# Kernel optimization log

Hardware: AMD Instinct MI355X
Metric: run time of the kernel (lower is better)

Reference implementation:

```python
import jax, jax.numpy as jnp
import numpy as np

EMBED_DIM = 1024
NUM_HEADS = 16
HEAD_DIM = EMBED_DIM // NUM_HEADS
ROPE_BASE = 10000.0


def rotate_half(x):
    # interleaved variant: pairs (x0,x1) -> (-x1, x0)
    x1 = x[..., ::2]
    x2 = x[..., 1::2]
    return jnp.stack((-x2, x1), axis=-1).reshape(x.shape)


def rope_tables(T, dim, dtype):
    inv_freq = 1.0 / (ROPE_BASE ** (jnp.arange(0, dim, 2, dtype=jnp.float32) / dim))
    t = jnp.arange(T, dtype=jnp.float32)
    freqs = t[:, None] * inv_freq[None, :]          # [T, dim/2]
    emb = jnp.concatenate((freqs, freqs), axis=-1)  # [T, dim]
    return jnp.cos(emb).astype(dtype), jnp.sin(emb).astype(dtype)


def setup_inputs() -> dict:
    key = jax.random.key(0)
    kx, kq, ko = jax.random.split(key, 3)
    B, T, D = 2, 2048, EMBED_DIM
    x = jax.random.normal(kx, (B, T, D), dtype=jnp.float32)
    s = 1.0 / np.sqrt(D)
    Wqkv = jax.random.normal(kq, (D, 3 * D), dtype=jnp.float32) * s
    Wout = jax.random.normal(ko, (D, D), dtype=jnp.float32) * s
    return {"x": x, "Wqkv": Wqkv, "Wout": Wout}


def reference(x, Wqkv, Wout):
    B, T, D = x.shape
    H, hd = NUM_HEADS, HEAD_DIM
    qkv = x @ Wqkv                                   # [B,T,3D]
    q, k, v = jnp.split(qkv, 3, axis=-1)
    q = q.reshape(B, T, H, hd).transpose(0, 2, 1, 3)  # [B,H,T,hd]
    k = k.reshape(B, T, H, hd).transpose(0, 2, 1, 3)
    v = v.reshape(B, T, H, hd).transpose(0, 2, 1, 3)
    cos, sin = rope_tables(T, hd, x.dtype)           # [T,hd]
    cos = cos[None, None, :, :]
    sin = sin[None, None, :, :]
    q = q * cos + rotate_half(q) * sin
    k = k * cos + rotate_half(k) * sin
    scale = 1.0 / np.sqrt(hd).astype(np.float32)
    attn = jnp.einsum('bhtd,bhsd->bhts', q, k) * scale  # [B,H,T,T]
    attn = jax.nn.softmax(attn, axis=-1)
    out = jnp.einsum('bhts,bhsd->bhtd', attn, v)     # [B,H,T,hd]
    out = out.transpose(0, 2, 1, 3).reshape(B, T, D)
    return out @ Wout
```

## Files before the change

kernel.cpp:

```cpp
#include <hip/hip_runtime.h>
#include <hip/hip_bf16.h>
#include <stdint.h>


typedef unsigned short u16;
typedef short bf16x8 __attribute__((ext_vector_type(8)));
typedef float f32x4  __attribute__((ext_vector_type(4)));

#if defined(__has_builtin) && __has_builtin(__builtin_amdgcn_exp2f)
#define EXP2F(x) __builtin_amdgcn_exp2f(x)
#else
#define EXP2F(x) exp2f(x)
#endif

__device__ __forceinline__ u16 f2b(float f) {
  uint32_t u = __float_as_uint(f);
  u += 0x7fffu + ((u >> 16) & 1u);
  return (u16)(u >> 16);
}
__device__ __forceinline__ uint32_t pk2(float a, float b) {
  return (uint32_t)f2b(a) | ((uint32_t)f2b(b) << 16);
}
__device__ __forceinline__ uint32_t pkbf(float a, float b) {
  __hip_bfloat162 h = __float22bfloat162_rn(make_float2(a, b));
  union { __hip_bfloat162 h2; uint32_t u; } cv; cv.h2 = h;
  return cv.u;
}

__device__ __forceinline__ void gl2lds16(const void* g, void* l) {
  __builtin_amdgcn_global_load_lds(
      (const __attribute__((address_space(1))) unsigned int*)g,
      (__attribute__((address_space(3))) unsigned int*)l, 16, 0, 0);
}

__global__ void sniff_kernel(const u16* x, int* flag) {
  __shared__ int cnt;
  if (threadIdx.x == 0) cnt = 0;
  __syncthreads();
  int c = 0;
  for (int i = threadIdx.x; i < 4096; i += 256) {
    float a = fabsf(__uint_as_float(((uint32_t)x[2*i]) << 16));
    if (a > 1e-3f && a < 100.f) c++;
  }
  atomicAdd(&cnt, c);
  __syncthreads();
  if (threadIdx.x == 0) *flag = (cnt > 2048) ? 1 : 0;
}

__device__ __forceinline__ void tr_tile(const void* src, u16* dst, int Kd, int N,
                                        int n0, int k0, int isb, u16* Lt, int tid)
{
  const int r = tid >> 2, cseg = (tid & 3) << 4;
  u16 t[16];
  if (isb) {
    const u16* s = (const u16*)src + (size_t)(k0 + r) * N + n0 + cseg;
    *(uint4*)&t[0] = *(const uint4*)s;
    *(uint4*)&t[8] = *(const uint4*)(s + 8);
  } else {
    const float* s = (const float*)src + (size_t)(k0 + r) * N + n0 + cseg;
    #pragma unroll
    for (int j = 0; j < 4; j++) {
      float4 v = *(const float4*)(s + j * 4);
      t[j*4+0] = f2b(v.x); t[j*4+1] = f2b(v.y); t[j*4+2] = f2b(v.z); t[j*4+3] = f2b(v.w);
    }
  }
  #pragma unroll
  for (int j = 0; j < 16; j++) Lt[(cseg + j) * 72 + r] = t[j];
  __syncthreads();
  const int n = tid >> 2, kseg = (tid & 3) << 4;
  uint4 u0 = *(const uint4*)&Lt[n * 72 + kseg];
  uint4 u1 = *(const uint4*)&Lt[n * 72 + kseg + 8];
  u16* d = dst + (size_t)(n0 + n) * Kd + k0 + kseg;
  *(uint4*)d = u0;
  *(uint4*)(d + 8) = u1;
}

__global__ __launch_bounds__(256) void prep_kernel(
    const void* __restrict__ x, const void* __restrict__ wqkv,
    const void* __restrict__ wout, const int* __restrict__ flag,
    u16* __restrict__ Xb, u16* __restrict__ Wqkvt, u16* __restrict__ Woutt,
    float2* __restrict__ CS)
{
  __shared__ u16 Lt[64 * 72];
  const int isb = *flag;
  const int bid = blockIdx.x, tid = threadIdx.x;
  if (bid < 2048) {
    const size_t i = ((size_t)bid * 256 + tid) * 8;
    if (isb) {
      *(uint4*)&Xb[i] = *(const uint4*)((const u16*)x + i);
    } else {
      const float* s = (const float*)x + i;
      float4 a = *(const float4*)s, b = *(const float4*)(s + 4);
      uint4 p;
      p.x = pkbf(a.x, a.y); p.y = pkbf(a.z, a.w);
      p.z = pkbf(b.x, b.y); p.w = pkbf(b.z, b.w);
      *(uint4*)&Xb[i] = p;
    }
  } else if (bid < 2816) {
    const int b = bid - 2048;
    tr_tile(wqkv, Wqkvt, 1024, 3072, (b % 48) * 64, (b / 48) * 64, isb, Lt, tid);
  } else if (bid < 3072) {
    const int b = bid - 2816;
    tr_tile(wout, Woutt, 1024, 1024, (b % 16) * 64, (b / 16) * 64, isb, Lt, tid);
  } else {
    const int idx = (bid - 3072) * 256 + tid;
    const int t = idx >> 5, f = idx & 31;
    float invf = __expf(-(float)f * 0.2878231366242557f);
    float th = (float)t * invf;
    float sn, cs;
    sincosf(th, &sn, &cs);
    CS[idx] = make_float2(cs, sn);
  }
}

__global__ __launch_bounds__(256) void qkv_kernel(
    const u16* __restrict__ Xb, const u16* __restrict__ Wt,
    const float2* __restrict__ CS,
    u16* __restrict__ Q, u16* __restrict__ K, u16* __restrict__ Vt)
{
  __shared__ u16 As[128 * 64];
  __shared__ u16 Bs[128 * 64];
  const int tid = threadIdx.x;
  const int n0 = blockIdx.x * 128;
  const int m0 = blockIdx.y * 128;
  const int w = tid >> 6, l = tid & 63, lr = l & 15, lq = l >> 4;
  const int mrow0 = (w & 1) * 64;
  const int ncol0 = (w >> 1) * 64;
  const int srow = tid >> 3;
  const int gseg = (tid & 7) ^ (srow & 7);

  f32x4 acc[4][4] = {};

  for (int k0 = 0; k0 < 1024; k0 += 64) {
    __syncthreads();
    #pragma unroll
    for (int rd = 0; rd < 4; rd++) {
      const int row = srow + rd * 32;
      gl2lds16(Xb + (size_t)(m0 + row) * 1024 + k0 + gseg * 8, &As[tid * 8 + rd * 2048]);
      gl2lds16(Wt + (size_t)(n0 + row) * 1024 + k0 + gseg * 8, &Bs[tid * 8 + rd * 2048]);
    }
    __syncthreads();
    #pragma unroll
    for (int kc = 0; kc < 2; kc++) {
      bf16x8 af[4], bf[4];
      #pragma unroll
      for (int i = 0; i < 4; i++) {
        const int seg = ((kc << 2) | lq) ^ (lr & 7);
        af[i] = *(const bf16x8*)&As[(mrow0 + i * 16 + lr) * 64 + seg * 8];
        bf[i] = *(const bf16x8*)&Bs[(ncol0 + i * 16 + lr) * 64 + seg * 8];
      }
      #pragma unroll
      for (int mb = 0; mb < 4; mb++)
        #pragma unroll
        for (int nb = 0; nb < 4; nb++)
          acc[mb][nb] = __builtin_amdgcn_mfma_f32_16x16x32_bf16(af[mb], bf[nb], acc[mb][nb], 0, 0, 0);
    }
  }

  const int col0 = n0 + ncol0;
  const int sec = col0 >> 10;
  const int h = (col0 >> 6) & 15;
  if (sec == 2) {
    #pragma unroll
    for (int mb = 0; mb < 4; mb++) {
      const int row0 = m0 + mrow0 + mb * 16 + lq * 4;
      const int b = row0 >> 11, t0 = row0 & 2047;
      #pragma unroll
      for (int nb = 0; nb < 4; nb++) {
        const int d = nb * 16 + lr;
        uint2 uv;
        uv.x = pkbf(acc[mb][nb][0], acc[mb][nb][1]);
        uv.y = pkbf(acc[mb][nb][2], acc[mb][nb][3]);
        *(uint2*)&Vt[(((size_t)b * 16 + h) * 64 + d) * 2048 + t0] = uv;
      }
    }
  } else {
    u16* dst = (sec == 0) ? Q : K;
    const float qscale = 0.125f * 1.44269504f;
    #pragma unroll
    for (int mb = 0; mb < 4; mb++) {
      const int row0 = m0 + mrow0 + mb * 16 + lq * 4;
      const int b = row0 >> 11, t0 = row0 & 2047;
      #pragma unroll
      for (int nb = 0; nb < 4; nb++) {
        const int d = nb * 16 + lr;
        const int f = d & 31;
        #pragma unroll
        for (int r = 0; r < 4; r++) {
          const int t = t0 + r;
          float2 cs = CS[t * 32 + f];
          float val = acc[mb][nb][r];
          float prt = __shfl_xor(val, 1, 64);
          float res = fmaf(val, cs.x, ((d & 1) ? prt : -prt) * cs.y);
          if (sec == 0) res *= qscale;
          dst[(((size_t)b * 16 + h) * 2048 + t) * 64 + d] = f2b(res);
        }
      }
    }
  }
}

__global__ __launch_bounds__(256, 2) void attn_kernel(
    const u16* __restrict__ Q, const u16* __restrict__ K,
    const u16* __restrict__ Vt, u16* __restrict__ ATT,
    float* __restrict__ Op, float* __restrict__ Ls)
{
  __shared__ u16 Ks[2][64 * 64];
  __shared__ u16 Vs[2][64 * 64];
  __shared__ u16 Ps[4][64 * 64];
  const int tid = threadIdx.x;
  const int w = tid >> 6, l = tid & 63, lr = l & 15, lq = l >> 4;
  const int bh = blockIdx.x >> 3;
  const int qt = blockIdx.x & 7;
  const int ns = gridDim.y, sh = blockIdx.y;
  const int slen = 2048 / ns;
  const int sbeg = sh * slen;
  const size_t base = (size_t)bh * (2048 * 64);
  const int qrow0 = qt * 256 + w * 64;
  u16* Psw = &Ps[w][0];

  bf16x8 qf[4][2];
  #pragma unroll
  for (int mb = 0; mb < 4; mb++)
    #pragma unroll
    for (int kc = 0; kc < 2; kc++)
      qf[mb][kc] = *(const bf16x8*)(Q + base + (size_t)(qrow0 + mb * 16 + lr) * 64 + kc * 32 + lq * 8);

  f32x4 oa[4][4] = {};
  float lsum[4] = {0.f, 0.f, 0.f, 0.f};

  const int srow = tid >> 3;

  auto stage = [&](int buf, int s0) {
    #pragma unroll
    for (int rd = 0; rd < 2; rd++) {
      const int row = srow + rd * 32;
      const int gs = (tid & 7) ^ (row & 7);
      gl2lds16(K + base + (size_t)(s0 + row) * 64 + gs * 8, &Ks[buf][tid * 8 + rd * 2048]);
      gl2lds16(Vt + base + (size_t)row * 2048 + s0 + gs * 8, &Vs[buf][tid * 8 + rd * 2048]);
    }
  };

  stage(0, sbeg);
  const int nt = slen >> 6;

  #pragma unroll 1
  for (int t = 0; t < nt; t++) {
    const int buf = t & 1;
    __syncthreads();
    if (t + 1 < nt) stage(buf ^ 1, sbeg + (t + 1) * 64);

    bf16x8 kf[4][2], vf[4][2];
    #pragma unroll
    for (int nb = 0; nb < 4; nb++)
      #pragma unroll
      for (int kc = 0; kc < 2; kc++) {
        const int seg = ((kc << 2) | lq) ^ (lr & 7);
        kf[nb][kc] = *(const bf16x8*)&Ks[buf][(nb * 16 + lr) * 64 + seg * 8];
        vf[nb][kc] = *(const bf16x8*)&Vs[buf][(nb * 16 + lr) * 64 + seg * 8];
      }

    #pragma unroll
    for (int sb = 0; sb < 4; sb++) {
      #pragma unroll
      for (int mb = 0; mb < 4; mb++) {
        f32x4 st = {};
        st = __builtin_amdgcn_mfma_f32_16x16x32_bf16(kf[sb][0], qf[mb][0], st, 0, 0, 0);
        st = __builtin_amdgcn_mfma_f32_16x16x32_bf16(kf[sb][1], qf[mb][1], st, 0, 0, 0);
        float e0 = EXP2F(st[0]), e1 = EXP2F(st[1]), e2 = EXP2F(st[2]), e3 = EXP2F(st[3]);
        lsum[mb] += (e0 + e1) + (e2 + e3);
        uint2 pp;
        pp.x = pkbf(e0, e1);
        pp.y = pkbf(e2, e3);
        const int pseg = ((sb << 1) | (lq >> 1)) ^ (lr & 7);
        *(uint2*)&Psw[(mb * 16 + lr) * 64 + pseg * 8 + (lq & 1) * 4] = pp;
      }
    }

    #pragma unroll
    for (int mb = 0; mb < 4; mb++) {
      const int rs0 = lq ^ (lr & 7);
      const int rs1 = (4 | lq) ^ (lr & 7);
      bf16x8 pf0 = *(const bf16x8*)&Psw[(mb * 16 + lr) * 64 + rs0 * 8];
      bf16x8 pf1 = *(const bf16x8*)&Psw[(mb * 16 + lr) * 64 + rs1 * 8];
      #pragma unroll
      for (int db = 0; db < 4; db++) {
        oa[db][mb] = __builtin_amdgcn_mfma_f32_16x16x32_bf16(vf[db][0], pf0, oa[db][mb], 0, 0, 0);
        oa[db][mb] = __builtin_amdgcn_mfma_f32_16x16x32_bf16(vf[db][1], pf1, oa[db][mb], 0, 0, 0);
      }
    }
  }

  #pragma unroll
  for (int mb = 0; mb < 4; mb++) {
    float v = lsum[mb];
    v += __shfl_xor(v, 16, 64);
    v += __shfl_xor(v, 32, 64);
    lsum[mb] = v;
  }

  const int b = bh >> 4, h = bh & 15;
  if (ns == 1) {
    #pragma unroll
    for (int mb = 0; mb < 4; mb++) {
      const float inv = 1.f / lsum[mb];
      const int t = qrow0 + mb * 16 + lr;
      u16* dst = ATT + ((size_t)(b * 2048 + t)) * 1024 + h * 64;
      #pragma unroll
      for (int db = 0; db < 4; db++) {
        uint2 u;
        u.x = pkbf(oa[db][mb][0] * inv, oa[db][mb][1] * inv);
        u.y = pkbf(oa[db][mb][2] * inv, oa[db][mb][3] * inv);
        *(uint2*)&dst[db * 16 + lq * 4] = u;
      }
    }
  } else {
    float* op = Op + (size_t)sh * (65536ull * 64);
    #pragma unroll
    for (int mb = 0; mb < 4; mb++) {
      const size_t row = (size_t)bh * 2048 + qrow0 + mb * 16 + lr;
      #pragma unroll
      for (int db = 0; db < 4; db++)
        *(f32x4*)&op[row * 64 + db * 16 + lq * 4] = oa[db][mb];
      if (lq == 0) Ls[(size_t)sh * 65536 + row] = lsum[mb];
    }
  }
}

__global__ __launch_bounds__(256) void combine_kernel(
    const float* __restrict__ Op, const float* __restrict__ Ls, u16* __restrict__ ATT)
{
  const int idx = blockIdx.x * 256 + threadIdx.x;
  const int R = idx >> 3;
  const int c = (idx & 7) * 8;
  const float* p0 = Op + (size_t)R * 64 + c;
  const float* p1 = p0 + 65536ull * 64;
  f32x4 a0 = *(const f32x4*)p0, a1 = *(const f32x4*)(p0 + 4);
  f32x4 b0 = *(const f32x4*)p1, b1 = *(const f32x4*)(p1 + 4);
  const float inv = 1.f / (Ls[R] + Ls[65536 + R]);
  const int bh = R >> 11, trow = R & 2047;
  const int b = bh >> 4, h = bh & 15;
  u16* d = ATT + ((size_t)(b * 2048 + trow)) * 1024 + h * 64 + c;
  uint4 u;
  u.x = pkbf((a0[0] + b0[0]) * inv, (a0[1] + b0[1]) * inv);
  u.y = pkbf((a0[2] + b0[2]) * inv, (a0[3] + b0[3]) * inv);
  u.z = pkbf((a1[0] + b1[0]) * inv, (a1[1] + b1[1]) * inv);
  u.w = pkbf((a1[2] + b1[2]) * inv, (a1[3] + b1[3]) * inv);
  *(uint4*)d = u;
}

__global__ __launch_bounds__(256) void outproj_kernel(
    const u16* __restrict__ A, const u16* __restrict__ Wt,
    const int* __restrict__ flag, void* __restrict__ outv)
{
  __shared__ u16 As[128 * 64];
  __shared__ u16 Bs[128 * 64];
  const int isb = *flag;
  const int tid = threadIdx.x;
  const int n0 = blockIdx.x * 128;
  const int m0 = blockIdx.y * 128;
  const int w = tid >> 6, l = tid & 63, lr = l & 15, lq = l >> 4;
  const int mrow0 = (w & 1) * 64;
  const int ncol0 = (w >> 1) * 64;
  const int srow = tid >> 3;
  const int gseg = (tid & 7) ^ (srow & 7);

  f32x4 acc[4][4] = {};

  for (int k0 = 0; k0 < 1024; k0 += 64) {
    __syncthreads();
    #pragma unroll
    for (int rd = 0; rd < 4; rd++) {
      const int row = srow + rd * 32;
      gl2lds16(A + (size_t)(m0 + row) * 1024 + k0 + gseg * 8, &As[tid * 8 + rd * 2048]);
      gl2lds16(Wt + (size_t)(n0 + row) * 1024 + k0 + gseg * 8, &Bs[tid * 8 + rd * 2048]);
    }
    __syncthreads();
    #pragma unroll
    for (int kc = 0; kc < 2; kc++) {
      bf16x8 af[4], bf[4];
      #pragma unroll
      for (int i = 0; i < 4; i++) {
        const int seg = ((kc << 2) | lq) ^ (lr & 7);
        af[i] = *(const bf16x8*)&As[(mrow0 + i * 16 + lr) * 64 + seg * 8];
        bf[i] = *(const bf16x8*)&Bs[(ncol0 + i * 16 + lr) * 64 + seg * 8];
      }
      #pragma unroll
      for (int mb = 0; mb < 4; mb++)
        #pragma unroll
        for (int nb = 0; nb < 4; nb++)
          acc[mb][nb] = __builtin_amdgcn_mfma_f32_16x16x32_bf16(af[mb], bf[nb], acc[mb][nb], 0, 0, 0);
    }
  }
  #pragma unroll
  for (int mb = 0; mb < 4; mb++) {
    const int row = m0 + mrow0 + mb * 16 + lq * 4;
    #pragma unroll
    for (int nb = 0; nb < 4; nb++) {
      const int col = n0 + ncol0 + nb * 16 + lr;
      #pragma unroll
      for (int r = 0; r < 4; r++) {
        float val = acc[mb][nb][r];
        if (isb) ((u16*)outv)[(size_t)(row + r) * 1024 + col] = f2b(val);
        else     ((float*)outv)[(size_t)(row + r) * 1024 + col] = val;
      }
    }
  }
}

extern "C" void kernel_launch(void* const* d_in, const int* in_sizes, int n_in,
                              void* d_out, int out_size, void* d_ws, size_t ws_size,
                              hipStream_t stream)
{
  const void* x    = d_in[0];
  const void* wqkv = d_in[1];
  const void* wout = d_in[2];
  char* ws = (char*)d_ws;
  const size_t MB = 1024 * 1024;
  int*    flag   = (int*)ws;
  float2* CS     = (float2*)(ws + 1024);
  u16*    Xb     = (u16*)(ws + 1 * MB);
  u16*    ATT    = Xb;
  u16*    Wqkvt  = (u16*)(ws + 9 * MB);
  u16*    Woutt  = (u16*)(ws + 15 * MB);
  u16*    Q      = (u16*)(ws + 17 * MB);
  u16*    K      = (u16*)(ws + 25 * MB);
  u16*    Vt     = (u16*)(ws + 33 * MB);
  float*  Op     = (float*)(ws + 41 * MB);
  float*  Ls     = (float*)(ws + 75 * MB);

  const bool split = ws_size >= 76 * MB;
  const int ns = split ? 2 : 1;

  sniff_kernel<<<1, 256, 0, stream>>>((const u16*)x, flag);
  prep_kernel<<<3328, 256, 0, stream>>>(x, wqkv, wout, flag, Xb, Wqkvt, Woutt, CS);
  qkv_kernel<<<dim3(24, 32), 256, 0, stream>>>(Xb, Wqkvt, CS, Q, K, Vt);
  attn_kernel<<<dim3(256, ns), 256, 0, stream>>>(Q, K, Vt, ATT, Op, Ls);
  if (split)
    combine_kernel<<<2048, 256, 0, stream>>>(Op, Ls, ATT);
  outproj_kernel<<<dim3(8, 32), 256, 0, stream>>>(ATT, Woutt, flag, d_out);
}
```

Baseline: 214.6 us.

## Keep softmax probabilities in registers and drop split-KV attention and sniff kernel

The attention kernel now feeds exponentiated scores straight into 16x16x16 MFMAs as register operands instead of writing P to LDS and reading it back. The 2-way KV split is removed, so the combine kernel and its fp32 partial buffers go away, and each block now covers 128 query rows over 512 blocks. The dtype-sniff kernel is folded into every block of the prep, qkv and outproj kernels, which lets bf16 inputs skip the X copy. The hardware exp2 builtin is replaced with exp2f. The trade-offs are smaller MFMAs with less K-depth per instruction, redundant sniff reads in every block, and less query reuse of each K/V tile per block.

```diff
diff --git a/kernel.cpp b/kernel.cpp
--- a/kernel.cpp
+++ b/kernel.cpp
@@ -5,22 +5,18 @@
 
 typedef unsigned short u16;
 typedef short bf16x8 __attribute__((ext_vector_type(8)));
+typedef short bf16x4 __attribute__((ext_vector_type(4)));
 typedef float f32x4  __attribute__((ext_vector_type(4)));
 
-#if defined(__has_builtin) && __has_builtin(__builtin_amdgcn_exp2f)
-#define EXP2F(x) __builtin_amdgcn_exp2f(x)
-#else
 #define EXP2F(x) exp2f(x)
-#endif
+
+#define MFMA16(a, b, c) __builtin_amdgcn_mfma_f32_16x16x16bf16_1k(a, b, c, 0, 0, 0)
 
 __device__ __forceinline__ u16 f2b(float f) {
   uint32_t u = __float_as_uint(f);
   u += 0x7fffu + ((u >> 16) & 1u);
   return (u16)(u >> 16);
 }
-__device__ __forceinline__ uint32_t pk2(float a, float b) {
-  return (uint32_t)f2b(a) | ((uint32_t)f2b(b) << 16);
-}
 __device__ __forceinline__ uint32_t pkbf(float a, float b) {
   __hip_bfloat162 h = __float22bfloat162_rn(make_float2(a, b));
   union { __hip_bfloat162 h2; uint32_t u; } cv; cv.h2 = h;
@@ -33,18 +29,17 @@
       (__attribute__((address_space(3))) unsigned int*)l, 16, 0, 0);
 }
 
-__global__ void sniff_kernel(const u16* x, int* flag) {
-  __shared__ int cnt;
-  if (threadIdx.x == 0) cnt = 0;
+__device__ __forceinline__ int sniff_local(const u16* x, int* scnt, int tid) {
+  if (tid == 0) *scnt = 0;
   __syncthreads();
   int c = 0;
-  for (int i = threadIdx.x; i < 4096; i += 256) {
-    float a = fabsf(__uint_as_float(((uint32_t)x[2*i]) << 16));
+  for (int i = tid; i < 4096; i += 256) {
+    float a = fabsf(__uint_as_float(((uint32_t)x[2 * i]) << 16));
     if (a > 1e-3f && a < 100.f) c++;
   }
-  atomicAdd(&cnt, c);
+  atomicAdd(scnt, c);
   __syncthreads();
-  if (threadIdx.x == 0) *flag = (cnt > 2048) ? 1 : 0;
+  return (*scnt > 2048) ? 1 : 0;
 }
 
 __device__ __forceinline__ void tr_tile(const void* src, u16* dst, int Kd, int N,
@@ -77,25 +72,23 @@
 
 __global__ __launch_bounds__(256) void prep_kernel(
     const void* __restrict__ x, const void* __restrict__ wqkv,
-    const void* __restrict__ wout, const int* __restrict__ flag,
+    const void* __restrict__ wout,
     u16* __restrict__ Xb, u16* __restrict__ Wqkvt, u16* __restrict__ Woutt,
     float2* __restrict__ CS)
 {
   __shared__ u16 Lt[64 * 72];
-  const int isb = *flag;
+  __shared__ int scnt;
   const int bid = blockIdx.x, tid = threadIdx.x;
+  const int isb = sniff_local((const u16*)x, &scnt, tid);
   if (bid < 2048) {
+    if (isb) return;
     const size_t i = ((size_t)bid * 256 + tid) * 8;
-    if (isb) {
-      *(uint4*)&Xb[i] = *(const uint4*)((const u16*)x + i);
-    } else {
-      const float* s = (const float*)x + i;
-      float4 a = *(const float4*)s, b = *(const float4*)(s + 4);
-      uint4 p;
-      p.x = pkbf(a.x, a.y); p.y = pkbf(a.z, a.w);
-      p.z = pkbf(b.x, b.y); p.w = pkbf(b.z, b.w);
-      *(uint4*)&Xb[i] = p;
-    }
+    const float* s = (const float*)x + i;
+    float4 a = *(const float4*)s, b = *(const float4*)(s + 4);
+    uint4 p;
+    p.x = pkbf(a.x, a.y); p.y = pkbf(a.z, a.w);
+    p.z = pkbf(b.x, b.y); p.w = pkbf(b.z, b.w);
+    *(uint4*)&Xb[i] = p;
   } else if (bid < 2816) {
     const int b = bid - 2048;
     tr_tile(wqkv, Wqkvt, 1024, 3072, (b % 48) * 64, (b / 48) * 64, isb, Lt, tid);
@@ -114,13 +107,16 @@
 }
 
 __global__ __launch_bounds__(256) void qkv_kernel(
-    const u16* __restrict__ Xb, const u16* __restrict__ Wt,
-    const float2* __restrict__ CS,
+    const void* __restrict__ xraw, const u16* __restrict__ Xb,
+    const u16* __restrict__ Wt, const float2* __restrict__ CS,
     u16* __restrict__ Q, u16* __restrict__ K, u16* __restrict__ Vt)
 {
   __shared__ u16 As[128 * 64];
   __shared__ u16 Bs[128 * 64];
+  __shared__ int scnt;
   const int tid = threadIdx.x;
+  const int isb = sniff_local((const u16*)xraw, &scnt, tid);
+  const u16* Asrc = isb ? (const u16*)xraw : Xb;
   const int n0 = blockIdx.x * 128;
   const int m0 = blockIdx.y * 128;
   const int w = tid >> 6, l = tid & 63, lr = l & 15, lq = l >> 4;
@@ -136,7 +132,7 @@
     #pragma unroll
     for (int rd = 0; rd < 4; rd++) {
       const int row = srow + rd * 32;
-      gl2lds16(Xb + (size_t)(m0 + row) * 1024 + k0 + gseg * 8, &As[tid * 8 + rd * 2048]);
+      gl2lds16(Asrc + (size_t)(m0 + row) * 1024 + k0 + gseg * 8, &As[tid * 8 + rd * 2048]);
       gl2lds16(Wt + (size_t)(n0 + row) * 1024 + k0 + gseg * 8, &Bs[tid * 8 + rd * 2048]);
     }
     __syncthreads();
@@ -202,32 +198,26 @@
 
 __global__ __launch_bounds__(256, 2) void attn_kernel(
     const u16* __restrict__ Q, const u16* __restrict__ K,
-    const u16* __restrict__ Vt, u16* __restrict__ ATT,
-    float* __restrict__ Op, float* __restrict__ Ls)
+    const u16* __restrict__ Vt, u16* __restrict__ ATT)
 {
   __shared__ u16 Ks[2][64 * 64];
   __shared__ u16 Vs[2][64 * 64];
-  __shared__ u16 Ps[4][64 * 64];
   const int tid = threadIdx.x;
   const int w = tid >> 6, l = tid & 63, lr = l & 15, lq = l >> 4;
-  const int bh = blockIdx.x >> 3;
-  const int qt = blockIdx.x & 7;
-  const int ns = gridDim.y, sh = blockIdx.y;
-  const int slen = 2048 / ns;
-  const int sbeg = sh * slen;
+  const int bh = blockIdx.x & 31;
+  const int qt = blockIdx.x >> 5;
   const size_t base = (size_t)bh * (2048 * 64);
-  const int qrow0 = qt * 256 + w * 64;
-  u16* Psw = &Ps[w][0];
-
-  bf16x8 qf[4][2];
+  const int qrow0 = qt * 128 + w * 32;
+
+  bf16x8 qf[2][2];
   #pragma unroll
-  for (int mb = 0; mb < 4; mb++)
+  for (int mb = 0; mb < 2; mb++)
     #pragma unroll
     for (int kc = 0; kc < 2; kc++)
       qf[mb][kc] = *(const bf16x8*)(Q + base + (size_t)(qrow0 + mb * 16 + lr) * 64 + kc * 32 + lq * 8);
 
-  f32x4 oa[4][4] = {};
-  float lsum[4] = {0.f, 0.f, 0.f, 0.f};
+  f32x4 oa[4][2] = {};
+  float2 ls2[2] = {};
 
   const int srow = tid >> 3;
 
@@ -241,122 +231,77 @@
     }
   };
 
-  stage(0, sbeg);
-  const int nt = slen >> 6;
+  stage(0, 0);
 
   #pragma unroll 1
-  for (int t = 0; t < nt; t++) {
+  for (int t = 0; t < 32; t++) {
     const int buf = t & 1;
     __syncthreads();
-    if (t + 1 < nt) stage(buf ^ 1, sbeg + (t + 1) * 64);
-
-    bf16x8 kf[4][2], vf[4][2];
-    #pragma unroll
-    for (int nb = 0; nb < 4; nb++)
+    if (t + 1 < 32) stage(buf ^ 1, (t + 1) * 64);
+
+    bf16x8 kf[4][2];
+    #pragma unroll
+    for (int sb = 0; sb < 4; sb++)
       #pragma unroll
       for (int kc = 0; kc < 2; kc++) {
         const int seg = ((kc << 2) | lq) ^ (lr & 7);
-        kf[nb][kc] = *(const bf16x8*)&Ks[buf][(nb * 16 + lr) * 64 + seg * 8];
-        vf[nb][kc] = *(const bf16x8*)&Vs[buf][(nb * 16 + lr) * 64 + seg * 8];
+        kf[sb][kc] = *(const bf16x8*)&Ks[buf][(sb * 16 + lr) * 64 + seg * 8];
       }
 
     #pragma unroll
     for (int sb = 0; sb < 4; sb++) {
-      #pragma unroll
-      for (int mb = 0; mb < 4; mb++) {
+      bf16x4 vf4[4];
+      #pragma unroll
+      for (int db = 0; db < 4; db++) {
+        const int vseg = (((sb << 1) | (lq >> 1)) ^ (lr & 7));
+        vf4[db] = *(const bf16x4*)&Vs[buf][(db * 16 + lr) * 64 + vseg * 8 + (lq & 1) * 4];
+      }
+      #pragma unroll
+      for (int mb = 0; mb < 2; mb++) {
         f32x4 st = {};
         st = __builtin_amdgcn_mfma_f32_16x16x32_bf16(kf[sb][0], qf[mb][0], st, 0, 0, 0);
         st = __builtin_amdgcn_mfma_f32_16x16x32_bf16(kf[sb][1], qf[mb][1], st, 0, 0, 0);
         float e0 = EXP2F(st[0]), e1 = EXP2F(st[1]), e2 = EXP2F(st[2]), e3 = EXP2F(st[3]);
-        lsum[mb] += (e0 + e1) + (e2 + e3);
-        uint2 pp;
-        pp.x = pkbf(e0, e1);
-        pp.y = pkbf(e2, e3);
-        const int pseg = ((sb << 1) | (lq >> 1)) ^ (lr & 7);
-        *(uint2*)&Psw[(mb * 16 + lr) * 64 + pseg * 8 + (lq & 1) * 4] = pp;
-      }
-    }
-
-    #pragma unroll
-    for (int mb = 0; mb < 4; mb++) {
-      const int rs0 = lq ^ (lr & 7);
-      const int rs1 = (4 | lq) ^ (lr & 7);
-      bf16x8 pf0 = *(const bf16x8*)&Psw[(mb * 16 + lr) * 64 + rs0 * 8];
-      bf16x8 pf1 = *(const bf16x8*)&Psw[(mb * 16 + lr) * 64 + rs1 * 8];
-      #pragma unroll
-      for (int db = 0; db < 4; db++) {
-        oa[db][mb] = __builtin_amdgcn_mfma_f32_16x16x32_bf16(vf[db][0], pf0, oa[db][mb], 0, 0, 0);
-        oa[db][mb] = __builtin_amdgcn_mfma_f32_16x16x32_bf16(vf[db][1], pf1, oa[db][mb], 0, 0, 0);
-      }
-    }
-  }
-
+        ls2[mb].x += e0 + e2;
+        ls2[mb].y += e1 + e3;
+        union { uint2 u; bf16x4 v; } pf;
+        pf.u.x = pkbf(e0, e1);
+        pf.u.y = pkbf(e2, e3);
+        #pragma unroll
+        for (int db = 0; db < 4; db++)
+          oa[db][mb] = MFMA16(vf4[db], pf.v, oa[db][mb]);
+      }
+    }
+  }
+
+  const int b = bh >> 4, h = bh & 15;
   #pragma unroll
-  for (int mb = 0; mb < 4; mb++) {
-    float v = lsum[mb];
+  for (int mb = 0; mb < 2; mb++) {
+    float v = ls2[mb].x + ls2[mb].y;
     v += __shfl_xor(v, 16, 64);
     v += __shfl_xor(v, 32, 64);
-    lsum[mb] = v;
-  }
-
-  const int b = bh >> 4, h = bh & 15;
-  if (ns == 1) {
-    #pragma unroll
-    for (int mb = 0; mb < 4; mb++) {
-      const float inv = 1.f / lsum[mb];
-      const int t = qrow0 + mb * 16 + lr;
-      u16* dst = ATT + ((size_t)(b * 2048 + t)) * 1024 + h * 64;
-      #pragma unroll
-      for (int db = 0; db < 4; db++) {
-        uint2 u;
-        u.x = pkbf(oa[db][mb][0] * inv, oa[db][mb][1] * inv);
-        u.y = pkbf(oa[db][mb][2] * inv, oa[db][mb][3] * inv);
-        *(uint2*)&dst[db * 16 + lq * 4] = u;
-      }
-    }
-  } else {
-    float* op = Op + (size_t)sh * (65536ull * 64);
-    #pragma unroll
-    for (int mb = 0; mb < 4; mb++) {
-      const size_t row = (size_t)bh * 2048 + qrow0 + mb * 16 + lr;
-      #pragma unroll
-      for (int db = 0; db < 4; db++)
-        *(f32x4*)&op[row * 64 + db * 16 + lq * 4] = oa[db][mb];
-      if (lq == 0) Ls[(size_t)sh * 65536 + row] = lsum[mb];
-    }
-  }
-}
-
-__global__ __launch_bounds__(256) void combine_kernel(
-    const float* __restrict__ Op, const float* __restrict__ Ls, u16* __restrict__ ATT)
-{
-  const int idx = blockIdx.x * 256 + threadIdx.x;
-  const int R = idx >> 3;
-  const int c = (idx & 7) * 8;
-  const float* p0 = Op + (size_t)R * 64 + c;
-  const float* p1 = p0 + 65536ull * 64;
-  f32x4 a0 = *(const f32x4*)p0, a1 = *(const f32x4*)(p0 + 4);
-  f32x4 b0 = *(const f32x4*)p1, b1 = *(const f32x4*)(p1 + 4);
-  const float inv = 1.f / (Ls[R] + Ls[65536 + R]);
-  const int bh = R >> 11, trow = R & 2047;
-  const int b = bh >> 4, h = bh & 15;
-  u16* d = ATT + ((size_t)(b * 2048 + trow)) * 1024 + h * 64 + c;
-  uint4 u;
-  u.x = pkbf((a0[0] + b0[0]) * inv, (a0[1] + b0[1]) * inv);
-  u.y = pkbf((a0[2] + b0[2]) * inv, (a0[3] + b0[3]) * inv);
-  u.z = pkbf((a1[0] + b1[0]) * inv, (a1[1] + b1[1]) * inv);
-  u.w = pkbf((a1[2] + b1[2]) * inv, (a1[3] + b1[3]) * inv);
-  *(uint4*)d = u;
+    const float inv = 1.f / v;
+    const int t = qrow0 + mb * 16 + lr;
+    u16* dst = ATT + ((size_t)(b * 2048 + t)) * 1024 + h * 64;
+    #pragma unroll
+    for (int db = 0; db < 4; db++) {
+      uint2 u;
+      u.x = pkbf(oa[db][mb][0] * inv, oa[db][mb][1] * inv);
+      u.y = pkbf(oa[db][mb][2] * inv, oa[db][mb][3] * inv);
+      *(uint2*)&dst[db * 16 + lq * 4] = u;
+    }
+  }
 }
 
 __global__ __launch_bounds__(256) void outproj_kernel(
     const u16* __restrict__ A, const u16* __restrict__ Wt,
-    const int* __restrict__ flag, void* __restrict__ outv)
+    const void* __restrict__ xraw, void* __restrict__ outv)
 {
   __shared__ u16 As[128 * 64];
   __shared__ u16 Bs[128 * 64];
-  const int isb = *flag;
+  __shared__ int scnt;
   const int tid = threadIdx.x;
+  const int isb = sniff_local((const u16*)xraw, &scnt, tid);
   const int n0 = blockIdx.x * 128;
   const int m0 = blockIdx.y * 128;
   const int w = tid >> 6, l = tid & 63, lr = l & 15, lq = l >> 4;
@@ -417,7 +362,6 @@
   const void* wout = d_in[2];
   char* ws = (char*)d_ws;
   const size_t MB = 1024 * 1024;
-  int*    flag   = (int*)ws;
   float2* CS     = (float2*)(ws + 1024);
   u16*    Xb     = (u16*)(ws + 1 * MB);
   u16*    ATT    = Xb;
@@ -426,17 +370,9 @@
   u16*    Q      = (u16*)(ws + 17 * MB);
   u16*    K      = (u16*)(ws + 25 * MB);
   u16*    Vt     = (u16*)(ws + 33 * MB);
-  float*  Op     = (float*)(ws + 41 * MB);
-  float*  Ls     = (float*)(ws + 75 * MB);
-
-  const bool split = ws_size >= 76 * MB;
-  const int ns = split ? 2 : 1;
-
-  sniff_kernel<<<1, 256, 0, stream>>>((const u16*)x, flag);
-  prep_kernel<<<3328, 256, 0, stream>>>(x, wqkv, wout, flag, Xb, Wqkvt, Woutt, CS);
-  qkv_kernel<<<dim3(24, 32), 256, 0, stream>>>(Xb, Wqkvt, CS, Q, K, Vt);
-  attn_kernel<<<dim3(256, ns), 256, 0, stream>>>(Q, K, Vt, ATT, Op, Ls);
-  if (split)
-    combine_kernel<<<2048, 256, 0, stream>>>(Op, Ls, ATT);
-  outproj_kernel<<<dim3(8, 32), 256, 0, stream>>>(ATT, Woutt, flag, d_out);
-}
+
+  prep_kernel<<<3328, 256, 0, stream>>>(x, wqkv, wout, Xb, Wqkvt, Woutt, CS);
+  qkv_kernel<<<dim3(24, 32), 256, 0, stream>>>(x, Xb, Wqkvt, CS, Q, K, Vt);
+  attn_kernel<<<512, 256, 0, stream>>>(Q, K, Vt, ATT);
+  outproj_kernel<<<dim3(8, 32), 256, 0, stream>>>(ATT, Woutt, x, d_out);
+}
```

After: 242.5 us. 13.0% more time.
